# Performance work log

Measured on AMD Instinct MI355X. Metric: run time of the kernel, lower is better.

The kernel has to match this reference:

```python
import jax, jax.numpy as jnp
import numpy as np

D_IN = 2048
D_OUT = 2048
NUM_HEADS = 16
NUM_GROUPS = 4
HEAD_DIM = D_OUT // NUM_HEADS          # 128
HEADS_PER_GROUP = NUM_HEADS // NUM_GROUPS  # 4


def setup_inputs() -> dict:
    key = jax.random.key(0)
    ks = jax.random.split(key, 6)
    b, s = 2, 2048
    x = jax.random.normal(ks[0], (b, s, D_IN), dtype=jnp.float32)
    # Store weights as [in, out] so y = x @ W (equivalent to torch Linear x @ W.T)
    sc_q = 1.0 / np.sqrt(D_IN)
    Wq = jax.random.uniform(ks[1], (D_IN, D_OUT), jnp.float32, -sc_q, sc_q)
    Wk = jax.random.uniform(ks[2], (D_IN, NUM_GROUPS * HEAD_DIM), jnp.float32, -sc_q, sc_q)
    Wv = jax.random.uniform(ks[3], (D_IN, NUM_GROUPS * HEAD_DIM), jnp.float32, -sc_q, sc_q)
    sc_o = 1.0 / np.sqrt(D_OUT)
    Wo = jax.random.uniform(ks[4], (D_OUT, D_OUT), jnp.float32, -sc_o, sc_o)
    bo = jax.random.uniform(ks[5], (D_OUT,), jnp.float32, -sc_o, sc_o)
    return {"x": x, "Wq": Wq, "Wk": Wk, "Wv": Wv, "Wo": Wo, "bo": bo}


def reference(x, Wq, Wk, Wv, Wo, bo):
    b, s, _ = x.shape
    g, hpg, hd = NUM_GROUPS, HEADS_PER_GROUP, HEAD_DIM
    # Projections; keep grouped layout instead of repeat_interleave (same math)
    q = (x @ Wq).reshape(b, s, g, hpg, hd)   # query heads ordered group-major,
                                             # matching repeat_interleave of K/V
    k = (x @ Wk).reshape(b, s, g, hd)
    v = (x @ Wv).reshape(b, s, g, hd)
    # scores: [b, g, hpg, q_len, k_len]
    scores = jnp.einsum('bqghd,bkgd->bghqk', q, k)
    causal = jnp.triu(jnp.ones((s, s), dtype=bool), k=1)  # True above diagonal
    scores = jnp.where(causal, -jnp.inf, scores)
    scale = 1.0 / jnp.sqrt(jnp.asarray(hd, dtype=scores.dtype))
    attn = jax.nn.softmax(scores * scale, axis=-1)
    ctx = jnp.einsum('bghqk,bkgd->bqghd', attn, v).reshape(b, s, D_OUT)
    return ctx @ Wo + bo
```

## Files before the change

### kernel.cpp

```cpp
#include <hip/hip_runtime.h>

typedef short v8s __attribute__((ext_vector_type(8)));
typedef float v4f __attribute__((ext_vector_type(4)));

__device__ __forceinline__ short f2bf(float f) {
  union { float f; unsigned u; } v; v.f = f;
  unsigned r = v.u + 0x7FFFu + ((v.u >> 16) & 1u);
  return (short)(r >> 16);
}

__device__ __forceinline__ void gll16(const short* g, short* l) {
  __builtin_amdgcn_global_load_lds(
      (const __attribute__((address_space(1))) void*)g,
      (__attribute__((address_space(3))) void*)l, 16, 0, 0);
}

__global__ void cast_f32_bf16(const float* __restrict__ in, short* __restrict__ out, int n4) {
  int i = blockIdx.x * blockDim.x + threadIdx.x;
  if (i >= n4) return;
  float4 v = ((const float4*)in)[i];
  short4 o;
  o.x = f2bf(v.x); o.y = f2bf(v.y); o.z = f2bf(v.z); o.w = f2bf(v.w);
  ((short4*)out)[i] = o;
}

__global__ void cast_transpose_weights(const float* __restrict__ Wq, const float* __restrict__ Wk,
                                       const float* __restrict__ Wv, const float* __restrict__ Wo,
                                       short* __restrict__ Wqkvt, short* __restrict__ Wot) {
  __shared__ float tile[32][33];
  const int tx = threadIdx.x, ty = threadIdx.y;
  int bx = blockIdx.x;
  const float* src; short* dst; int C, cb;
  if (bx < 64)      { src = Wq; dst = Wqkvt;                        C = 2048; cb = bx; }
  else if (bx < 80) { src = Wk; dst = Wqkvt + (size_t)2048 * 2048;  C = 512;  cb = bx - 64; }
  else if (bx < 96) { src = Wv; dst = Wqkvt + (size_t)2560 * 2048;  C = 512;  cb = bx - 80; }
  else              { src = Wo; dst = Wot;                          C = 2048; cb = bx - 96; }
  const int c0 = cb * 32, r0 = blockIdx.y * 32;
#pragma unroll
  for (int i = 0; i < 4; ++i)
    tile[ty + 8 * i][tx] = src[(size_t)(r0 + ty + 8 * i) * C + c0 + tx];
  __syncthreads();
#pragma unroll
  for (int i = 0; i < 4; ++i)
    dst[(size_t)(c0 + ty + 8 * i) * 2048 + r0 + tx] = f2bf(tile[tx][ty + 8 * i]);
}

__global__ void transpose_v_perm(const short* __restrict__ qkv, short* __restrict__ out) {
  __shared__ short tile[32][33];
  const int tx = threadIdx.x, ty = threadIdx.y;
  const int c0 = blockIdx.x * 32, r0 = blockIdx.y * 32;
  const int z = blockIdx.z;
#pragma unroll
  for (int i = 0; i < 4; ++i)
    tile[ty + 8 * i][tx] = qkv[(size_t)(z * 2048 + r0 + ty + 8 * i) * 3072 + 2560 + c0 + tx];
  __syncthreads();
#pragma unroll
  for (int i = 0; i < 4; ++i) {
    int k = r0 + tx;
    int pk = (k & ~31) | ((((k >> 2) & 3) * 2 + ((k >> 4) & 1)) * 4) | (k & 3);
    out[(size_t)z * 512 * 2048 + (size_t)(c0 + ty + 8 * i) * 2048 + pk] = tile[tx][ty + 8 * i];
  }
}

template <int BF16_OUT>
__global__ __launch_bounds__(256) void gemm_bt(const short* __restrict__ A,
                                               const short* __restrict__ Bt,
                                               void* __restrict__ Cout,
                                               const float* __restrict__ bias,
                                               int M, int N, int K) {
  __shared__ short As[128 * 32];
  __shared__ short Bs[128 * 32];
  const int tid = threadIdx.x;
  const int m0 = blockIdx.y * 128, n0 = blockIdx.x * 128;
  const int w = tid >> 6, lane = tid & 63, quad = lane >> 4, l16 = lane & 15;
  const int wm = (w >> 1) * 64, wn = (w & 1) * 64;
  v4f acc[4][4] = {};
  const int srow = lane >> 2, scol = (lane & 3) * 8;
  const short* Ap = A + (size_t)(m0 + w * 32 + srow) * K + scol;
  const short* Bp = Bt + (size_t)(n0 + w * 32 + srow) * K + scol;
  short* AsW = &As[(w * 32) * 32 + lane * 8];
  short* BsW = &Bs[(w * 32) * 32 + lane * 8];
  const size_t rstep = (size_t)16 * K;
  for (int k0 = 0; k0 < K; k0 += 32) {
    __syncthreads();
    gll16(Ap, AsW);
    gll16(Ap + rstep, AsW + 16 * 32);
    gll16(Bp, BsW);
    gll16(Bp + rstep, BsW + 16 * 32);
    __syncthreads();
    Ap += 32; Bp += 32;
    v8s af[4], bf[4];
#pragma unroll
    for (int i = 0; i < 4; ++i) af[i] = *(const v8s*)&As[(wm + i * 16 + l16) * 32 + quad * 8];
#pragma unroll
    for (int i = 0; i < 4; ++i) bf[i] = *(const v8s*)&Bs[(wn + i * 16 + l16) * 32 + quad * 8];
#pragma unroll
    for (int mi = 0; mi < 4; ++mi)
#pragma unroll
      for (int ni = 0; ni < 4; ++ni)
        acc[mi][ni] = __builtin_amdgcn_mfma_f32_16x16x32_bf16(af[mi], bf[ni], acc[mi][ni], 0, 0, 0);
  }
#pragma unroll
  for (int mi = 0; mi < 4; ++mi) {
#pragma unroll
    for (int ni = 0; ni < 4; ++ni) {
      const int col = n0 + wn + ni * 16 + l16;
#pragma unroll
      for (int r = 0; r < 4; ++r) {
        const int row = m0 + wm + mi * 16 + quad * 4 + r;
        if (BF16_OUT) {
          ((short*)Cout)[(size_t)row * N + col] = f2bf(acc[mi][ni][r]);
        } else {
          ((float*)Cout)[(size_t)row * N + col] = acc[mi][ni][r] + bias[col];
        }
      }
    }
  }
}

__global__ __launch_bounds__(256, 2) void flash_attn4(const short* __restrict__ QKV,
                                                      const short* __restrict__ Vtb,
                                                      short* __restrict__ ctx) {
  __shared__ __align__(16) short smem[32768];
  const int tid = threadIdx.x;
  const int w = tid >> 6, lane = tid & 63, quad = lane >> 4, l16 = lane & 15;
  const int wq = w >> 1, wk = w & 1;
  const int bh = blockIdx.y;
  const int b = bh >> 4, h = bh & 15, g = h >> 2;
  const float scale = 0.08838834764831845f;
  v8s ones;
#pragma unroll
  for (int i = 0; i < 8; ++i) ones[i] = (short)0x3F80;

  const int krl = lane >> 4, kcl = lane & 15;
  const int vrl = lane >> 3, vcl = lane & 7;
  const short* Kg0 = QKV + (size_t)(b * 2048 + w * 16 + krl) * 3072 + 2048 + g * 128;
  const short* Vg0 = Vtb + (size_t)(b * 512 + g * 128 + w * 32 + vrl) * 2048 + (vcl ^ (vrl & 7)) * 8;
  short* kd = smem + (w * 16) * 128 + lane * 8;
  short* vd = smem + 8192 + (w * 32) * 64 + lane * 8;

  auto stage = [&](int key0, int bs) {
    const short* kg = Kg0 + (size_t)key0 * 3072;
    const short* vg = Vg0 + key0;
#pragma unroll
    for (int ii = 0; ii < 4; ++ii) {
      const int rl = (ii * 4 + krl) & 15;
      gll16(kg + (size_t)(ii * 4) * 3072 + (kcl ^ rl) * 8, kd + bs * 16384 + ii * 512);
      gll16(vg + (size_t)(ii * 8) * 2048, vd + bs * 16384 + ii * 512);
    }
  };

  float* red = (float*)smem;

#pragma unroll 1
  for (int half = 0; half < 2; ++half) {
    const int qt = half ? (31 - blockIdx.x) : blockIdx.x;
    const int q0 = qt * 64;
    const int qb = q0 + wq * 32;

    v8s aq[2][4];
#pragma unroll
    for (int qs = 0; qs < 2; ++qs) {
      const short* Qp = QKV + (size_t)(b * 2048 + qb + qs * 16 + l16) * 3072 + h * 128 + quad * 8;
#pragma unroll
      for (int kk = 0; kk < 4; ++kk) aq[qs][kk] = *(const v8s*)(Qp + kk * 32);
    }
    v4f o[2][8] = {};
    v4f ol[2] = {};

    __syncthreads();
    stage(0, 0);
    const int nk = qt + 1;
#pragma unroll 1
    for (int kt = 0; kt < nk; ++kt) {
      const int key0 = kt << 6;
      __syncthreads();
      if (kt + 1 < nk) stage((kt + 1) << 6, (kt + 1) & 1);
      const short* Ks = smem + (kt & 1) * 16384;
      const short* Vs = Ks + 8192;
      const int kb = key0 + wk * 32;
      if (kb > qb + 31) continue;
      v4f sf[2][2] = {};
#pragma unroll
      for (int kfl = 0; kfl < 2; ++kfl)
#pragma unroll
        for (int kk = 0; kk < 4; ++kk) {
          v8s kfr = *(const v8s*)&Ks[((wk * 2 + kfl) * 16 + l16) * 128 + (((kk * 4 + quad) ^ l16) * 8)];
#pragma unroll
          for (int qs = 0; qs < 2; ++qs)
            sf[qs][kfl] = __builtin_amdgcn_mfma_f32_16x16x32_bf16(kfr, aq[qs][kk], sf[qs][kfl], 0, 0, 0);
        }
      const bool diag = (kb + 31 > qb);
      v8s pa[2];
#pragma unroll
      for (int qs = 0; qs < 2; ++qs) {
        const int qg = qb + qs * 16 + l16;
        v8s t;
#pragma unroll
        for (int kfl = 0; kfl < 2; ++kfl)
#pragma unroll
          for (int r = 0; r < 4; ++r) {
            float s = sf[qs][kfl][r] * scale;
            if (diag && (kb + kfl * 16 + quad * 4 + r > qg)) s = -1e30f;
            t[kfl * 4 + r] = f2bf(__expf(s));
          }
        pa[qs] = t;
      }
#pragma unroll
      for (int nf = 0; nf < 8; ++nf) {
        v8s vf = *(const v8s*)&Vs[(nf * 16 + l16) * 64 + (((wk * 4 + quad) ^ (l16 & 7)) * 8)];
#pragma unroll
        for (int qs = 0; qs < 2; ++qs)
          o[qs][nf] = __builtin_amdgcn_mfma_f32_16x16x32_bf16(pa[qs], vf, o[qs][nf], 0, 0, 0);
      }
#pragma unroll
      for (int qs = 0; qs < 2; ++qs)
        ol[qs] = __builtin_amdgcn_mfma_f32_16x16x32_bf16(pa[qs], ones, ol[qs], 0, 0, 0);
    }
    __syncthreads();

    if (wk == 1) {
#pragma unroll
      for (int qs = 0; qs < 2; ++qs)
        *(v4f*)&red[(wq * 2 + qs) * 256 + l16 * 16 + quad * 4] = ol[qs];
    }
    __syncthreads();
    if (wk == 0) {
#pragma unroll
      for (int qs = 0; qs < 2; ++qs)
        ol[qs] += *(const v4f*)&red[(wq * 2 + qs) * 256 + l16 * 16 + quad * 4];
    }
    __syncthreads();
    if (wk == 1) {
#pragma unroll
      for (int qs = 0; qs < 2; ++qs)
#pragma unroll
        for (int nf = 0; nf < 8; ++nf)
          *(v4f*)&red[(((wq * 2 + qs) * 8 + nf) * 256) + l16 * 16 + quad * 4] = o[qs][nf];
    }
    __syncthreads();
    if (wk == 0) {
#pragma unroll
      for (int qs = 0; qs < 2; ++qs) {
        float inv[4];
#pragma unroll
        for (int r = 0; r < 4; ++r) inv[r] = 1.0f / ol[qs][r];
#pragma unroll
        for (int nf = 0; nf < 8; ++nf) {
          v4f osum = o[qs][nf] + *(const v4f*)&red[(((wq * 2 + qs) * 8 + nf) * 256) + l16 * 16 + quad * 4];
#pragma unroll
          for (int r = 0; r < 4; ++r) {
            const int row = qb + qs * 16 + quad * 4 + r;
            ctx[(size_t)(b * 2048 + row) * 2048 + h * 128 + nf * 16 + l16] = f2bf(osum[r] * inv[r]);
          }
        }
      }
    }
  }
}

extern "C" void kernel_launch(void* const* d_in, const int* in_sizes, int n_in,
                              void* d_out, int out_size, void* d_ws, size_t ws_size,
                              hipStream_t stream) {
  const float* x = (const float*)d_in[0];
  const float* Wq = (const float*)d_in[1];
  const float* Wk = (const float*)d_in[2];
  const float* Wv = (const float*)d_in[3];
  const float* Wo = (const float*)d_in[4];
  const float* bo = (const float*)d_in[5];
  float* out = (float*)d_out;
  char* ws = (char*)d_ws;

  short* xb    = (short*)(ws);
  short* ctx   = (short*)(ws);
  short* Wqkvt = (short*)(ws + 16777216);
  short* Wot   = (short*)(ws + 29360128);
  short* QKV   = (short*)(ws + 37748736);
  short* Vtb   = (short*)(ws + 62914560);

  dim3 tb(32, 8);
  cast_f32_bf16<<<8192, 256, 0, stream>>>(x, xb, 2097152);
  cast_transpose_weights<<<dim3(160, 64), tb, 0, stream>>>(Wq, Wk, Wv, Wo, Wqkvt, Wot);

  gemm_bt<1><<<dim3(24, 32), 256, 0, stream>>>(xb, Wqkvt, (void*)QKV, nullptr, 4096, 3072, 2048);

  transpose_v_perm<<<dim3(16, 64, 2), tb, 0, stream>>>(QKV, Vtb);

  flash_attn4<<<dim3(16, 32), 256, 0, stream>>>(QKV, Vtb, ctx);

  gemm_bt<0><<<dim3(16, 32), 256, 0, stream>>>(ctx, Wot, (void*)out, bo, 4096, 2048, 2048);
}
```

Measured before the change: 300.4 us.

## Double-buffer GEMM with swizzled LDS, XCD block remap, fused cast kernels, MFMA priority

The GEMM becomes a double-buffered kernel that prefetches the next K-tile while computing the current one, cutting the barriers per iteration from two to one. It also XOR-swizzles LDS columns to avoid bank conflicts and remaps block IDs so neighbouring tiles land on the same XCD, which should help L2 reuse. The two cast kernels merge into one launch, and s_setprio is raised around MFMA sections in both the GEMM and the attention kernel. The cost is twice the LDS per GEMM block, which is meant to fit three blocks per CU via launch_bounds.

```diff
diff --git a/kernel.cpp b/kernel.cpp
--- a/kernel.cpp
+++ b/kernel.cpp
@@ -15,27 +15,31 @@
       (__attribute__((address_space(3))) void*)l, 16, 0, 0);
 }
 
-__global__ void cast_f32_bf16(const float* __restrict__ in, short* __restrict__ out, int n4) {
-  int i = blockIdx.x * blockDim.x + threadIdx.x;
-  if (i >= n4) return;
-  float4 v = ((const float4*)in)[i];
-  short4 o;
-  o.x = f2bf(v.x); o.y = f2bf(v.y); o.z = f2bf(v.z); o.w = f2bf(v.w);
-  ((short4*)out)[i] = o;
-}
-
-__global__ void cast_transpose_weights(const float* __restrict__ Wq, const float* __restrict__ Wk,
-                                       const float* __restrict__ Wv, const float* __restrict__ Wo,
-                                       short* __restrict__ Wqkvt, short* __restrict__ Wot) {
+__global__ void cast_and_transpose(const float* __restrict__ x, short* __restrict__ xb,
+                                   const float* __restrict__ Wq, const float* __restrict__ Wk,
+                                   const float* __restrict__ Wv, const float* __restrict__ Wo,
+                                   short* __restrict__ Wqkvt, short* __restrict__ Wot) {
+  const int tid = threadIdx.x;
+  int bid = blockIdx.x;
+  if (bid < 8192) {
+    int i = bid * 256 + tid;
+    float4 v = ((const float4*)x)[i];
+    short4 o;
+    o.x = f2bf(v.x); o.y = f2bf(v.y); o.z = f2bf(v.z); o.w = f2bf(v.w);
+    ((short4*)xb)[i] = o;
+    return;
+  }
   __shared__ float tile[32][33];
-  const int tx = threadIdx.x, ty = threadIdx.y;
-  int bx = blockIdx.x;
+  bid -= 8192;
+  const int tx = tid & 31, ty = tid >> 5;
+  int bx = bid % 160;
+  const int byy = bid / 160;
   const float* src; short* dst; int C, cb;
   if (bx < 64)      { src = Wq; dst = Wqkvt;                        C = 2048; cb = bx; }
   else if (bx < 80) { src = Wk; dst = Wqkvt + (size_t)2048 * 2048;  C = 512;  cb = bx - 64; }
   else if (bx < 96) { src = Wv; dst = Wqkvt + (size_t)2560 * 2048;  C = 512;  cb = bx - 80; }
   else              { src = Wo; dst = Wot;                          C = 2048; cb = bx - 96; }
-  const int c0 = cb * 32, r0 = blockIdx.y * 32;
+  const int c0 = cb * 32, r0 = byy * 32;
 #pragma unroll
   for (int i = 0; i < 4; ++i)
     tile[ty + 8 * i][tx] = src[(size_t)(r0 + ty + 8 * i) * C + c0 + tx];
@@ -63,43 +67,65 @@
 }
 
 template <int BF16_OUT>
-__global__ __launch_bounds__(256) void gemm_bt(const short* __restrict__ A,
-                                               const short* __restrict__ Bt,
-                                               void* __restrict__ Cout,
-                                               const float* __restrict__ bias,
-                                               int M, int N, int K) {
-  __shared__ short As[128 * 32];
-  __shared__ short Bs[128 * 32];
+__global__ __launch_bounds__(256, 3) void gemm_bt2p(const short* __restrict__ A,
+                                                    const short* __restrict__ Bt,
+                                                    void* __restrict__ Cout,
+                                                    const float* __restrict__ bias,
+                                                    int N, int K, int nbx, int cpx) {
+  __shared__ __align__(16) short sm[2 * 8192];
   const int tid = threadIdx.x;
-  const int m0 = blockIdx.y * 128, n0 = blockIdx.x * 128;
   const int w = tid >> 6, lane = tid & 63, quad = lane >> 4, l16 = lane & 15;
   const int wm = (w >> 1) * 64, wn = (w & 1) * 64;
+  const int bid = blockIdx.x;
+  const int swz = (bid & 7) * cpx + (bid >> 3);
+  const int n0 = (swz % nbx) * 128, m0 = (swz / nbx) * 128;
+  const int NT = K >> 5;
+
+  const int srow = lane >> 2;
+  const int sc = ((lane & 3) ^ ((lane >> 2) & 3) ^ ((lane >> 4) & 3)) * 8;
+  const short* Ag = A + (size_t)(m0 + w * 16 + srow) * K + sc;
+  const short* Bg = Bt + (size_t)(n0 + w * 16 + srow) * K + sc;
+  short* Ad = sm + w * 512 + lane * 8;
+  short* Bd = sm + 4096 + w * 512 + lane * 8;
+  const size_t rjump = (size_t)64 * K;
+
+  auto stage = [&](int t, int bf_) {
+    const int k = t << 5;
+    short* ad = Ad + bf_ * 8192;
+    short* bd = Bd + bf_ * 8192;
+    gll16(Ag + k, ad);
+    gll16(Ag + k + rjump, ad + 2048);
+    gll16(Bg + k, bd);
+    gll16(Bg + k + rjump, bd + 2048);
+  };
+
+  const int rsc = (quad ^ (l16 & 3) ^ ((l16 >> 2) & 3)) * 8;
+  const short* aBase = sm + (wm + l16) * 32 + rsc;
+  const short* bBase = sm + 4096 + (wn + l16) * 32 + rsc;
+
   v4f acc[4][4] = {};
-  const int srow = lane >> 2, scol = (lane & 3) * 8;
-  const short* Ap = A + (size_t)(m0 + w * 32 + srow) * K + scol;
-  const short* Bp = Bt + (size_t)(n0 + w * 32 + srow) * K + scol;
-  short* AsW = &As[(w * 32) * 32 + lane * 8];
-  short* BsW = &Bs[(w * 32) * 32 + lane * 8];
-  const size_t rstep = (size_t)16 * K;
-  for (int k0 = 0; k0 < K; k0 += 32) {
-    __syncthreads();
-    gll16(Ap, AsW);
-    gll16(Ap + rstep, AsW + 16 * 32);
-    gll16(Bp, BsW);
-    gll16(Bp + rstep, BsW + 16 * 32);
-    __syncthreads();
-    Ap += 32; Bp += 32;
+
+  stage(0, 0);
+  __syncthreads();
+
+  for (int t = 0; t < NT; ++t) {
+    if (t + 1 < NT) stage(t + 1, (t + 1) & 1);
+    const int bo_ = (t & 1) * 8192;
     v8s af[4], bf[4];
 #pragma unroll
-    for (int i = 0; i < 4; ++i) af[i] = *(const v8s*)&As[(wm + i * 16 + l16) * 32 + quad * 8];
-#pragma unroll
-    for (int i = 0; i < 4; ++i) bf[i] = *(const v8s*)&Bs[(wn + i * 16 + l16) * 32 + quad * 8];
+    for (int i = 0; i < 4; ++i) af[i] = *(const v8s*)(aBase + bo_ + i * 512);
+#pragma unroll
+    for (int i = 0; i < 4; ++i) bf[i] = *(const v8s*)(bBase + bo_ + i * 512);
+    __builtin_amdgcn_s_setprio(1);
 #pragma unroll
     for (int mi = 0; mi < 4; ++mi)
 #pragma unroll
       for (int ni = 0; ni < 4; ++ni)
         acc[mi][ni] = __builtin_amdgcn_mfma_f32_16x16x32_bf16(af[mi], bf[ni], acc[mi][ni], 0, 0, 0);
-  }
+    __builtin_amdgcn_s_setprio(0);
+    if (t + 1 < NT) __syncthreads();
+  }
+
 #pragma unroll
   for (int mi = 0; mi < 4; ++mi) {
 #pragma unroll
@@ -181,6 +207,7 @@
       const int kb = key0 + wk * 32;
       if (kb > qb + 31) continue;
       v4f sf[2][2] = {};
+      __builtin_amdgcn_s_setprio(1);
 #pragma unroll
       for (int kfl = 0; kfl < 2; ++kfl)
 #pragma unroll
@@ -190,6 +217,7 @@
           for (int qs = 0; qs < 2; ++qs)
             sf[qs][kfl] = __builtin_amdgcn_mfma_f32_16x16x32_bf16(kfr, aq[qs][kk], sf[qs][kfl], 0, 0, 0);
         }
+      __builtin_amdgcn_s_setprio(0);
       const bool diag = (kb + 31 > qb);
       v8s pa[2];
 #pragma unroll
@@ -206,6 +234,7 @@
           }
         pa[qs] = t;
       }
+      __builtin_amdgcn_s_setprio(1);
 #pragma unroll
       for (int nf = 0; nf < 8; ++nf) {
         v8s vf = *(const v8s*)&Vs[(nf * 16 + l16) * 64 + (((wk * 4 + quad) ^ (l16 & 7)) * 8)];
@@ -216,6 +245,7 @@
 #pragma unroll
       for (int qs = 0; qs < 2; ++qs)
         ol[qs] = __builtin_amdgcn_mfma_f32_16x16x32_bf16(pa[qs], ones, ol[qs], 0, 0, 0);
+      __builtin_amdgcn_s_setprio(0);
     }
     __syncthreads();
 
@@ -278,15 +308,13 @@
   short* QKV   = (short*)(ws + 37748736);
   short* Vtb   = (short*)(ws + 62914560);
 
-  dim3 tb(32, 8);
-  cast_f32_bf16<<<8192, 256, 0, stream>>>(x, xb, 2097152);
-  cast_transpose_weights<<<dim3(160, 64), tb, 0, stream>>>(Wq, Wk, Wv, Wo, Wqkvt, Wot);
-
-  gemm_bt<1><<<dim3(24, 32), 256, 0, stream>>>(xb, Wqkvt, (void*)QKV, nullptr, 4096, 3072, 2048);
-
-  transpose_v_perm<<<dim3(16, 64, 2), tb, 0, stream>>>(QKV, Vtb);
+  cast_and_transpose<<<18432, 256, 0, stream>>>(x, xb, Wq, Wk, Wv, Wo, Wqkvt, Wot);
+
+  gemm_bt2p<1><<<768, 256, 0, stream>>>(xb, Wqkvt, (void*)QKV, nullptr, 3072, 2048, 24, 96);
+
+  transpose_v_perm<<<dim3(16, 64, 2), dim3(32, 8), 0, stream>>>(QKV, Vtb);
 
   flash_attn4<<<dim3(16, 32), 256, 0, stream>>>(QKV, Vtb, ctx);
 
-  gemm_bt<0><<<dim3(16, 32), 256, 0, stream>>>(ctx, Wot, (void*)out, bo, 4096, 2048, 2048);
-}
+  gemm_bt2p<0><<<512, 256, 0, stream>>>(ctx, Wot, (void*)out, bo, 2048, 2048, 16, 64);
+}
```

Result: faster. 288.9 us (-3.8%).
